# Kernel tuning notes

Measured on AMD Instinct MI355X. Metric: run time of the kernel, lower is better.

## Reference

```python
import jax, jax.numpy as jnp
import numpy as np

COMMITMENT = 1.0

def setup_inputs() -> dict:
    key = jax.random.key(0)
    k1, k2 = jax.random.split(key)
    x = jax.random.normal(k1, (32, 64, 64, 64), dtype=jnp.float32)       # [B, D, H, W]
    emb_w = jax.random.normal(k2, (512, 64), dtype=jnp.float32)          # [K, D] codebook
    return {"x": x, "emb_w": emb_w}

def reference(x, emb_w):
    B, D, H, W = x.shape
    K = emb_w.shape[0]
    # permute channels last and flatten: [B*H*W, D]
    xp = jnp.transpose(x, (0, 2, 3, 1))
    flat = xp.reshape(-1, D)
    # squared-distance matrix [N, K] via ||a||^2 + ||b||^2 - 2 a.b
    distances = (jnp.sum(flat * flat, axis=1, keepdims=True)
                 + jnp.sum(emb_w * emb_w, axis=1)
                 - 2.0 * jnp.matmul(flat, emb_w.T))
    encoding_flat = jnp.argmin(distances, axis=1)                        # [N]
    quantized = emb_w[encoding_flat].reshape(B, H, W, D)                 # gather
    quantized = jnp.transpose(quantized, (0, 3, 1, 2))                   # back to [B, D, H, W]
    # commitment loss: mse(stop_grad(quantized), x)
    e_latent_loss = jnp.mean((jax.lax.stop_gradient(quantized) - x) ** 2)
    loss = COMMITMENT * e_latent_loss
    # straight-through estimator
    quantized_st = x + jax.lax.stop_gradient(quantized - x)
    encoding = encoding_flat.reshape(B, H, W)
    return quantized_st, encoding, distances, loss
```

## Files before the change

### kernel.cpp

```cpp
#include <hip/hip_runtime.h>

typedef short short8 __attribute__((ext_vector_type(8)));
typedef float f32x4 __attribute__((ext_vector_type(4)));

#define EPS 0.012f

__device__ __forceinline__ unsigned short rne_bf16(float v) {
    unsigned u = __float_as_uint(v);
    unsigned r = u + 0x7FFFu + ((u >> 16) & 1u);
    return (unsigned short)(r >> 16);
}
__device__ __forceinline__ float bf16_to_f(unsigned short h) {
    return __uint_as_float(((unsigned)h) << 16);
}

#define MFMA(a,b,c) __builtin_amdgcn_mfma_f32_16x16x32_bf16((a),(b),(c),0,0,0)

__global__ __launch_bounds__(64) void prep_kernel(
    const float* __restrict__ emb, unsigned short* __restrict__ whi,
    unsigned short* __restrict__ wlo, float* __restrict__ wee)
{
    const int k = blockIdx.x * 64 + threadIdx.x;
    const float* src = emb + k * 64;
    float nrm = 0.f;
    #pragma unroll
    for (int g = 0; g < 8; ++g) {
        float4 v0 = *(const float4*)(src + g * 8);
        float4 v1 = *(const float4*)(src + g * 8 + 4);
        float vv[8] = {v0.x, v0.y, v0.z, v0.w, v1.x, v1.y, v1.z, v1.w};
        short8 h8, l8;
        #pragma unroll
        for (int i = 0; i < 8; ++i) {
            nrm = fmaf(vv[i], vv[i], nrm);
            unsigned short hb = rne_bf16(vv[i]);
            h8[i] = (short)hb;
            l8[i] = (short)rne_bf16(vv[i] - bf16_to_f(hb));
        }
        *(short8*)(whi + k * 64 + g * 8) = h8;
        *(short8*)(wlo + k * 64 + g * 8) = l8;
    }
    wee[k] = nrm;
}

__global__ __launch_bounds__(256, 4) void vq_kernel(
    const float* __restrict__ x, const float* __restrict__ emb,
    const unsigned short* __restrict__ whi, const unsigned short* __restrict__ wlo,
    const float* __restrict__ wee,
    float* __restrict__ out_q, float* __restrict__ out_enc,
    float* __restrict__ out_dist, float* __restrict__ out_loss)
{
    __shared__ __align__(16) unsigned short ehi[2][64 * 64];
    __shared__ __align__(16) unsigned short elo[2][64 * 64];
    __shared__ float ee_s[512];
    __shared__ int   enc_s[64];
    __shared__ float red_s[4];

    const int t   = threadIdx.x;
    const int bid = blockIdx.x;
    const int n_base = bid * 64;
    const size_t xbase = (size_t)(bid >> 6) * 262144 + (size_t)(bid & 63) * 64;
    const int l  = t & 63;
    const int wv = t >> 6;

    ee_s[t]       = wee[t];
    ee_s[t + 256] = wee[t + 256];

    const int myw = wv * 16 + (l & 15);
    const int g8  = (l >> 4) * 8;
    float va[16];
    {
        const float* xp = x + xbase + myw;
        #pragma unroll
        for (int i = 0; i < 8; ++i) {
            va[i]     = xp[(size_t)(g8 + i) * 4096];
            va[8 + i] = xp[(size_t)(g8 + 32 + i) * 4096];
        }
    }
    short8 xhi0, xhi1, xlo0, xlo1;
    float xx = 0.f;
    #pragma unroll
    for (int i = 0; i < 8; ++i) {
        xx = fmaf(va[i], va[i], xx);
        xx = fmaf(va[8 + i], va[8 + i], xx);
        unsigned short hb = rne_bf16(va[i]);
        xhi0[i] = (short)hb; xlo0[i] = (short)rne_bf16(va[i] - bf16_to_f(hb));
        unsigned short hb2 = rne_bf16(va[8 + i]);
        xhi1[i] = (short)hb2; xlo1[i] = (short)rne_bf16(va[8 + i] - bf16_to_f(hb2));
    }
    xx += __shfl_xor(xx, 16, 64);
    xx += __shfl_xor(xx, 32, 64);

    short8 sh[2], sl[2];
    #define STAGE_LOAD(c) {                                                   \
        _Pragma("unroll")                                                     \
        for (int p = 0; p < 2; ++p) {                                         \
            int u = t + p * 256;                                              \
            int kr = u >> 3, d0 = (u & 7) * 8;                                \
            sh[p] = *(const short8*)(whi + (size_t)(((c) * 64 + kr) * 64 + d0)); \
            sl[p] = *(const short8*)(wlo + (size_t)(((c) * 64 + kr) * 64 + d0)); \
        } }
    #define STAGE_WRITE(bufi) {                                               \
        _Pragma("unroll")                                                     \
        for (int p = 0; p < 2; ++p) {                                         \
            int u = t + p * 256;                                              \
            int kr = u >> 3, d0 = (u & 7) * 8;                                \
            int idx = kr * 64 + (d0 ^ ((kr & 7) << 3));                       \
            *(short8*)&ehi[bufi][idx] = sh[p];                                \
            *(short8*)&elo[bufi][idx] = sl[p];                                \
        } }

    STAGE_LOAD(0); STAGE_WRITE(0);
    float m1 = 3.4e38f, m2 = 3.4e38f; int k1 = 0;
    const int colb = (l >> 4) * 4;
    float* drow = out_dist + (size_t)(n_base + myw) * 512;
    __syncthreads();

    #pragma unroll 1
    for (int c = 0; c < 8; ++c) {
        if (c < 7) STAGE_LOAD(c + 1);
        const int bufi = c & 1;
        #pragma unroll
        for (int kti = 0; kti < 4; ++kti) {
            const int krl = kti * 16 + (l & 15);
            const int sw  = (krl & 7) << 3;
            const int bix = krl * 64;
            short8 ch0 = *(short8*)&ehi[bufi][bix + (g8 ^ sw)];
            short8 ch1 = *(short8*)&ehi[bufi][bix + ((g8 + 32) ^ sw)];
            short8 cl0 = *(short8*)&elo[bufi][bix + (g8 ^ sw)];
            short8 cl1 = *(short8*)&elo[bufi][bix + ((g8 + 32) ^ sw)];
            f32x4 accA = {0.f, 0.f, 0.f, 0.f};
            f32x4 accB = {0.f, 0.f, 0.f, 0.f};
            accA = MFMA(ch0, xhi0, accA);
            accB = MFMA(ch1, xhi1, accB);
            accA = MFMA(cl0, xhi0, accA);
            accB = MFMA(cl1, xhi1, accB);
            accA = MFMA(ch0, xlo0, accA);
            accB = MFMA(ch1, xlo1, accB);
            const int kb = c * 64 + kti * 16 + colb;
            float4 ee4 = *(const float4*)&ee_s[kb];
            float eev[4] = {ee4.x, ee4.y, ee4.z, ee4.w};
            f32x4 dist4;
            #pragma unroll
            for (int r = 0; r < 4; ++r) {
                float dv = fmaf(accA[r] + accB[r], -2.f, xx + eev[r]);
                dist4[r] = dv;
                if (dv < m1) { m2 = m1; m1 = dv; k1 = kb + r; }
                else if (dv < m2) m2 = dv;
            }
            *(f32x4*)(drow + kb) = dist4;
        }
        if (c < 7) STAGE_WRITE((c + 1) & 1);
        __syncthreads();
    }

    float bv = m1; int bk = k1;
    {
        float ov = __shfl_xor(bv, 16, 64); int ok = __shfl_xor(bk, 16, 64);
        if (ov < bv || (ov == bv && ok < bk)) { bv = ov; bk = ok; }
        ov = __shfl_xor(bv, 32, 64); ok = __shfl_xor(bk, 32, 64);
        if (ov < bv || (ov == bv && ok < bk)) { bv = ov; bk = ok; }
    }
    const float thr = bv + EPS;
    const unsigned long long gmask = 0x0001000100010001ULL << (l & 15);
    unsigned long long b1 = __ballot(m1 <= thr);
    unsigned long long b2 = __ballot(m2 <= thr);
    int enc = bk; float lossv = bv;
    if (__popcll(b1 & gmask) > 1 || (b2 & gmask) != 0ULL) {
        const float* dr   = drow + (l >> 4) * 128;
        const float* xcol = x + xbase + myw;
        double bestv = 1e300; int bestk = 0x7fffffff;
        #pragma unroll 1
        for (int c4 = 0; c4 < 32; ++c4) {
            float4 dv4 = *(const float4*)(dr + c4 * 4);
            float dvv[4] = {dv4.x, dv4.y, dv4.z, dv4.w};
            #pragma unroll 1
            for (int j = 0; j < 4; ++j) {
                if (dvv[j] <= thr) {
                    int k = (l >> 4) * 128 + c4 * 4 + j;
                    const float* er = emb + k * 64;
                    double s = 0.0;
                    #pragma unroll 4
                    for (int d = 0; d < 64; ++d) {
                        double df = (double)xcol[(size_t)d * 4096] - (double)er[d];
                        s += df * df;
                    }
                    if (s < bestv) { bestv = s; bestk = k; }
                }
            }
        }
        double ov = __shfl_xor(bestv, 16, 64); int ok = __shfl_xor(bestk, 16, 64);
        if (ov < bestv || (ov == bestv && ok < bestk)) { bestv = ov; bestk = ok; }
        ov = __shfl_xor(bestv, 32, 64); ok = __shfl_xor(bestk, 32, 64);
        if (ov < bestv || (ov == bestv && ok < bestk)) { bestv = ov; bestk = ok; }
        enc = bestk;
        if (l < 16 && enc != bk) lossv = drow[enc];
    }
    if (l < 16) {
        enc_s[myw] = enc;
        out_enc[n_base + myw] = (float)enc;
    }
    float lc = (l < 16) ? lossv : 0.f;
    #pragma unroll
    for (int m = 32; m >= 1; m >>= 1) lc += __shfl_down(lc, m, 64);
    if (l == 0) red_s[wv] = lc;
    __syncthreads();
    if (t == 0)
        atomicAdd(out_loss, (red_s[0] + red_s[1] + red_s[2] + red_s[3]) * (1.0f / 8388608.0f));

    {
        const int w  = t & 63;
        const int dg = t >> 6;
        const int e  = enc_s[w];
        const float* er = emb + e * 64 + dg * 16;
        float* qp = out_q + xbase + (size_t)(dg * 16) * 4096 + w;
        #pragma unroll
        for (int qi = 0; qi < 4; ++qi) {
            float4 q4 = *(const float4*)(er + qi * 4);
            qp[(size_t)(qi * 4 + 0) * 4096] = q4.x;
            qp[(size_t)(qi * 4 + 1) * 4096] = q4.y;
            qp[(size_t)(qi * 4 + 2) * 4096] = q4.z;
            qp[(size_t)(qi * 4 + 3) * 4096] = q4.w;
        }
    }
}

extern "C" void kernel_launch(void* const* d_in, const int* in_sizes, int n_in,
                              void* d_out, int out_size, void* d_ws, size_t ws_size,
                              hipStream_t stream) {
    const float* x   = (const float*)d_in[0];
    const float* emb = (const float*)d_in[1];

    float* out_q    = (float*)d_out;
    float* out_enc  = out_q + 8388608;
    float* out_dist = out_enc + 131072;
    float* out_loss = out_dist + 67108864;

    unsigned short* whi = (unsigned short*)d_ws;
    unsigned short* wlo = whi + 32768;
    float*          wee = (float*)(whi + 65536);

    hipMemsetAsync(out_loss, 0, sizeof(float), stream);
    prep_kernel<<<8, 64, 0, stream>>>(emb, whi, wlo, wee);
    vq_kernel<<<2048, 256, 0, stream>>>(x, emb, whi, wlo, wee,
                                        out_q, out_enc, out_dist, out_loss);
}
```

Baseline: 117.5 us.

## Stage distance tiles through LDS for coalesced stores; halve codebook chunk size

```diff
diff --git a/kernel.cpp b/kernel.cpp
--- a/kernel.cpp
+++ b/kernel.cpp
@@ -42,6 +42,8 @@
     wee[k] = nrm;
 }
 
+#define DT 36
+
 __global__ __launch_bounds__(256, 4) void vq_kernel(
     const float* __restrict__ x, const float* __restrict__ emb,
     const unsigned short* __restrict__ whi, const unsigned short* __restrict__ wlo,
@@ -49,8 +51,9 @@
     float* __restrict__ out_q, float* __restrict__ out_enc,
     float* __restrict__ out_dist, float* __restrict__ out_loss)
 {
-    __shared__ __align__(16) unsigned short ehi[2][64 * 64];
-    __shared__ __align__(16) unsigned short elo[2][64 * 64];
+    __shared__ __align__(16) unsigned short ehi[2][32 * 64];
+    __shared__ __align__(16) unsigned short elo[2][32 * 64];
+    __shared__ __align__(16) float dtile[4][16 * DT];
     __shared__ float ee_s[512];
     __shared__ int   enc_s[64];
     __shared__ float red_s[4];
@@ -90,37 +93,31 @@
     xx += __shfl_xor(xx, 16, 64);
     xx += __shfl_xor(xx, 32, 64);
 
-    short8 sh[2], sl[2];
-    #define STAGE_LOAD(c) {                                                   \
-        _Pragma("unroll")                                                     \
-        for (int p = 0; p < 2; ++p) {                                         \
-            int u = t + p * 256;                                              \
-            int kr = u >> 3, d0 = (u & 7) * 8;                                \
-            sh[p] = *(const short8*)(whi + (size_t)(((c) * 64 + kr) * 64 + d0)); \
-            sl[p] = *(const short8*)(wlo + (size_t)(((c) * 64 + kr) * 64 + d0)); \
-        } }
-    #define STAGE_WRITE(bufi) {                                               \
-        _Pragma("unroll")                                                     \
-        for (int p = 0; p < 2; ++p) {                                         \
-            int u = t + p * 256;                                              \
-            int kr = u >> 3, d0 = (u & 7) * 8;                                \
-            int idx = kr * 64 + (d0 ^ ((kr & 7) << 3));                       \
-            *(short8*)&ehi[bufi][idx] = sh[p];                                \
-            *(short8*)&elo[bufi][idx] = sl[p];                                \
-        } }
+    short8 sh, sl;
+    const int skr = t >> 3;
+    const int sd0 = (t & 7) * 8;
+    const int sidx = skr * 64 + (sd0 ^ ((skr & 7) << 3));
+    #define STAGE_LOAD(c) {                                                    \
+        sh = *(const short8*)(whi + (size_t)(((c) * 32 + skr) * 64 + sd0));    \
+        sl = *(const short8*)(wlo + (size_t)(((c) * 32 + skr) * 64 + sd0));    \
+    }
+    #define STAGE_WRITE(bufi) {                                                \
+        *(short8*)&ehi[bufi][sidx] = sh;                                       \
+        *(short8*)&elo[bufi][sidx] = sl;                                       \
+    }
 
     STAGE_LOAD(0); STAGE_WRITE(0);
     float m1 = 3.4e38f, m2 = 3.4e38f; int k1 = 0;
     const int colb = (l >> 4) * 4;
-    float* drow = out_dist + (size_t)(n_base + myw) * 512;
+    float* dwv = dtile[wv];
     __syncthreads();
 
     #pragma unroll 1
-    for (int c = 0; c < 8; ++c) {
-        if (c < 7) STAGE_LOAD(c + 1);
+    for (int c = 0; c < 16; ++c) {
+        if (c < 15) STAGE_LOAD(c + 1);
         const int bufi = c & 1;
         #pragma unroll
-        for (int kti = 0; kti < 4; ++kti) {
+        for (int kti = 0; kti < 2; ++kti) {
             const int krl = kti * 16 + (l & 15);
             const int sw  = (krl & 7) << 3;
             const int bix = krl * 64;
@@ -136,7 +133,7 @@
             accB = MFMA(cl1, xhi1, accB);
             accA = MFMA(ch0, xlo0, accA);
             accB = MFMA(ch1, xlo1, accB);
-            const int kb = c * 64 + kti * 16 + colb;
+            const int kb = c * 32 + kti * 16 + colb;
             float4 ee4 = *(const float4*)&ee_s[kb];
             float eev[4] = {ee4.x, ee4.y, ee4.z, ee4.w};
             f32x4 dist4;
@@ -147,12 +144,22 @@
                 if (dv < m1) { m2 = m1; m1 = dv; k1 = kb + r; }
                 else if (dv < m2) m2 = dv;
             }
-            *(f32x4*)(drow + kb) = dist4;
-        }
-        if (c < 7) STAGE_WRITE((c + 1) & 1);
+            *(f32x4*)&dwv[(l & 15) * DT + (kti * 4 + (l >> 4)) * 4] = dist4;
+        }
+        #pragma unroll
+        for (int p = 0; p < 2; ++p) {
+            const int row = p * 8 + (l >> 3);
+            const int k4  = (l & 7) * 4;
+            f32x4 v = *(f32x4*)&dwv[row * DT + k4];
+            *(f32x4*)(out_dist + (size_t)(n_base + wv * 16 + row) * 512 + c * 32 + k4) = v;
+        }
+        if (c < 15) STAGE_WRITE((c + 1) & 1);
         __syncthreads();
     }
 
+    __syncthreads();
+
+    float* drow = out_dist + (size_t)(n_base + myw) * 512;
     float bv = m1; int bk = k1;
     {
         float ov = __shfl_xor(bv, 16, 64); int ok = __shfl_xor(bk, 16, 64);
```

New measurement: 105.1 us. -10.6%, faster.
